# Optimization experiments

Hardware: AMD Instinct MI355X
Metric: run time of the kernel (lower is better)

The kernel has to match this reference:

```python
import jax, jax.numpy as jnp
import numpy as np

D_MODEL = 768
CODEBOOK_SIZE = 2048
CODEBOOK_DIM = 64


def setup_inputs() -> dict:
    key = jax.random.key(0)
    ks = jax.random.split(key, 10)
    B, N = 16, 4096
    h = CODEBOOK_DIM * 2  # 128
    def lin_init(k, fan_in, shape):
        bound = 1.0 / np.sqrt(fan_in)
        return jax.random.uniform(k, shape, jnp.float32, -bound, bound)
    inp = {
        "x": jax.random.normal(ks[0], (B, N, D_MODEL), jnp.float32),
        # encoder: Linear(d_model -> 2*cd), GELU, Linear(2*cd -> cd)
        "enc_w1": lin_init(ks[1], D_MODEL, (D_MODEL, h)),
        "enc_b1": lin_init(ks[2], D_MODEL, (h,)),
        "enc_w2": lin_init(ks[3], h, (h, CODEBOOK_DIM)),
        "enc_b2": lin_init(ks[4], h, (CODEBOOK_DIM,)),
        # codebook: uniform(-1/K, 1/K)
        "codebook": jax.random.uniform(ks[5], (CODEBOOK_SIZE, CODEBOOK_DIM), jnp.float32,
                                        -1.0 / CODEBOOK_SIZE, 1.0 / CODEBOOK_SIZE),
        # decoder: Linear(cd -> 2*cd), GELU, Linear(2*cd -> d_model)
        "dec_w1": lin_init(ks[6], CODEBOOK_DIM, (CODEBOOK_DIM, h)),
        "dec_b1": lin_init(ks[7], CODEBOOK_DIM, (h,)),
        "dec_w2": lin_init(ks[8], h, (h, D_MODEL)),
        "dec_b2": lin_init(ks[9], h, (D_MODEL,)),
    }
    return inp


def reference(x, enc_w1, enc_b1, enc_w2, enc_b2, codebook, dec_w1, dec_b1, dec_w2, dec_b2):
    B, N, _ = x.shape
    # encoder MLP (exact GELU, matching torch default)
    z = jax.nn.gelu(x @ enc_w1 + enc_b1, approximate=False) @ enc_w2 + enc_b2  # (B,N,cd)
    # quantize: squared-distance argmin over codebook
    flat_z = z.reshape(-1, CODEBOOK_DIM)  # (BN, cd)
    dist = (jnp.sum(flat_z * flat_z, axis=1, keepdims=True)
            + jnp.sum(codebook * codebook, axis=1)[None, :]
            - 2.0 * flat_z @ codebook.T)  # (BN, K)
    indices = jnp.argmin(dist, axis=-1)  # (BN,)
    z_q = codebook[indices].reshape(B, N, CODEBOOK_DIM)
    codebook_loss = jnp.mean((jax.lax.stop_gradient(z_q) - z) ** 2)
    embedding_loss = jnp.mean((z_q - jax.lax.stop_gradient(z)) ** 2)
    vq_loss = codebook_loss + 0.25 * embedding_loss
    # straight-through estimator
    z_q = z + jax.lax.stop_gradient(z_q - z)
    # decoder MLP
    x_rec = jax.nn.gelu(z_q @ dec_w1 + dec_b1, approximate=False) @ dec_w2 + dec_b2
    return x_rec, indices.reshape(B, N), vq_loss
```

## Files before the change

kernel.cpp:

```cpp
#include <hip/hip_runtime.h>
#include <math.h>

#define TOKENS 65536
#define DMODEL 768
#define HDIM 128
#define CDIM 64
#define NCODE 2048

__device__ __forceinline__ float gelu_exact(float v) {
    return 0.5f * v * (1.0f + erff(v * 0.7071067811865476f));
}

__device__ __forceinline__ void load_lds16(const float* g, float* l) {
    __builtin_amdgcn_global_load_lds(
        (const __attribute__((address_space(1))) void*)g,
        (__attribute__((address_space(3))) void*)l, 16, 0, 0);
}

__global__ __launch_bounds__(256) __attribute__((amdgpu_waves_per_eu(4, 4)))
void enc_fused(const float* __restrict__ x, const float* __restrict__ w1,
               const float* __restrict__ b1, const float* __restrict__ w2,
               const float* __restrict__ b2, float* __restrict__ Z)
{
    __shared__ union {
        float Wbuf[2][32][128];
        float H1s[64][132];
    } u;

    const int t = threadIdx.x;
    const int w = t >> 6, l = t & 63;
    const size_t tok0 = (size_t)blockIdx.x * 64;
    const int tg = t >> 5;
    const int cg = t & 31;

    float acc[8][4];
    #pragma unroll
    for (int i = 0; i < 8; ++i)
        #pragma unroll
        for (int j = 0; j < 4; ++j) acc[i][j] = 0.f;

    const float* xbase[8];
    #pragma unroll
    for (int i = 0; i < 8; ++i)
        xbase[i] = x + (tok0 + tg + 8 * i) * DMODEL;

    const int wrow_ = l >> 5;
    const int wcol_ = 4 * (l & 31);

    #define STAGE_W(buf, k0s)                                              \
        {                                                                  \
            float* dst = &u.Wbuf[buf][0][0];                               \
            _Pragma("unroll")                                              \
            for (int j = 0; j < 4; ++j) {                                  \
                const int chunk = w * 4 + j;                               \
                const int row = chunk * 2 + wrow_;                         \
                load_lds16(w1 + (size_t)((k0s) + row) * HDIM + wcol_,      \
                           dst + chunk * 256);                             \
            }                                                              \
        }

    STAGE_W(0, 0);
    __syncthreads();

    for (int tile = 0; tile < 24; ++tile) {
        const int k0 = tile * 32;
        const int cur = tile & 1;
        if (tile + 1 < 24) STAGE_W(cur ^ 1, k0 + 32);
        const float(*Wc)[128] = u.Wbuf[cur];
        #pragma unroll
        for (int kk = 0; kk < 32; kk += 4) {
            float4 av[8];
            #pragma unroll
            for (int i = 0; i < 8; ++i)
                av[i] = *reinterpret_cast<const float4*>(xbase[i] + k0 + kk);
            float4 bv[4];
            #pragma unroll
            for (int q = 0; q < 4; ++q)
                bv[q] = *reinterpret_cast<const float4*>(&Wc[kk + q][cg * 4]);
            #pragma unroll
            for (int i = 0; i < 8; ++i) {
                acc[i][0] = fmaf(av[i].x, bv[0].x, acc[i][0]);
                acc[i][1] = fmaf(av[i].x, bv[0].y, acc[i][1]);
                acc[i][2] = fmaf(av[i].x, bv[0].z, acc[i][2]);
                acc[i][3] = fmaf(av[i].x, bv[0].w, acc[i][3]);
                acc[i][0] = fmaf(av[i].y, bv[1].x, acc[i][0]);
                acc[i][1] = fmaf(av[i].y, bv[1].y, acc[i][1]);
                acc[i][2] = fmaf(av[i].y, bv[1].z, acc[i][2]);
                acc[i][3] = fmaf(av[i].y, bv[1].w, acc[i][3]);
                acc[i][0] = fmaf(av[i].z, bv[2].x, acc[i][0]);
                acc[i][1] = fmaf(av[i].z, bv[2].y, acc[i][1]);
                acc[i][2] = fmaf(av[i].z, bv[2].z, acc[i][2]);
                acc[i][3] = fmaf(av[i].z, bv[2].w, acc[i][3]);
                acc[i][0] = fmaf(av[i].w, bv[3].x, acc[i][0]);
                acc[i][1] = fmaf(av[i].w, bv[3].y, acc[i][1]);
                acc[i][2] = fmaf(av[i].w, bv[3].z, acc[i][2]);
                acc[i][3] = fmaf(av[i].w, bv[3].w, acc[i][3]);
            }
        }
        __syncthreads();
    }

    {
        float4 b1v = *reinterpret_cast<const float4*>(b1 + cg * 4);
        #pragma unroll
        for (int i = 0; i < 8; ++i) {
            float4 h;
            h.x = gelu_exact(acc[i][0] + b1v.x);
            h.y = gelu_exact(acc[i][1] + b1v.y);
            h.z = gelu_exact(acc[i][2] + b1v.z);
            h.w = gelu_exact(acc[i][3] + b1v.w);
            *reinterpret_cast<float4*>(&u.H1s[tg + 8 * i][cg * 4]) = h;
        }
    }
    __syncthreads();

    const int tg2 = t >> 4;
    const int cg2 = t & 15;
    const float4* w2_4 = reinterpret_cast<const float4*>(w2);
    float accB[4][4];
    #pragma unroll
    for (int i = 0; i < 4; ++i)
        #pragma unroll
        for (int j = 0; j < 4; ++j) accB[i][j] = 0.f;

    float4 bvn[4];
    #pragma unroll
    for (int q = 0; q < 4; ++q) bvn[q] = w2_4[(size_t)q * 16 + cg2];

    for (int k = 0; k < HDIM; k += 4) {
        float4 bv[4];
        #pragma unroll
        for (int q = 0; q < 4; ++q) bv[q] = bvn[q];
        if (k + 4 < HDIM) {
            #pragma unroll
            for (int q = 0; q < 4; ++q)
                bvn[q] = w2_4[(size_t)(k + 4 + q) * 16 + cg2];
        }
        float4 av[4];
        #pragma unroll
        for (int i = 0; i < 4; ++i)
            av[i] = *reinterpret_cast<const float4*>(&u.H1s[tg2 + 16 * i][k]);
        #pragma unroll
        for (int i = 0; i < 4; ++i) {
            accB[i][0] = fmaf(av[i].x, bv[0].x, accB[i][0]);
            accB[i][1] = fmaf(av[i].x, bv[0].y, accB[i][1]);
            accB[i][2] = fmaf(av[i].x, bv[0].z, accB[i][2]);
            accB[i][3] = fmaf(av[i].x, bv[0].w, accB[i][3]);
            accB[i][0] = fmaf(av[i].y, bv[1].x, accB[i][0]);
            accB[i][1] = fmaf(av[i].y, bv[1].y, accB[i][1]);
            accB[i][2] = fmaf(av[i].y, bv[1].z, accB[i][2]);
            accB[i][3] = fmaf(av[i].y, bv[1].w, accB[i][3]);
            accB[i][0] = fmaf(av[i].z, bv[2].x, accB[i][0]);
            accB[i][1] = fmaf(av[i].z, bv[2].y, accB[i][1]);
            accB[i][2] = fmaf(av[i].z, bv[2].z, accB[i][2]);
            accB[i][3] = fmaf(av[i].z, bv[2].w, accB[i][3]);
            accB[i][0] = fmaf(av[i].w, bv[3].x, accB[i][0]);
            accB[i][1] = fmaf(av[i].w, bv[3].y, accB[i][1]);
            accB[i][2] = fmaf(av[i].w, bv[3].z, accB[i][2]);
            accB[i][3] = fmaf(av[i].w, bv[3].w, accB[i][3]);
        }
    }
    {
        float4 b2v = *reinterpret_cast<const float4*>(b2 + cg2 * 4);
        #pragma unroll
        for (int i = 0; i < 4; ++i) {
            float4 o;
            o.x = accB[i][0] + b2v.x;
            o.y = accB[i][1] + b2v.y;
            o.z = accB[i][2] + b2v.z;
            o.w = accB[i][3] + b2v.w;
            *reinterpret_cast<float4*>(Z + (tok0 + tg2 + 16 * i) * CDIM + cg2 * 4) = o;
        }
    }
    #undef STAGE_W
}

__global__ __launch_bounds__(256)
void vq_kernel(const float* __restrict__ Z, const float* __restrict__ cb,
               const float* __restrict__ cnorm, int* __restrict__ idx_out,
               float* __restrict__ idxf_out, float* __restrict__ loss_accum)
{
    __shared__ float Zs[64][68];
    __shared__ float CsT[64][128];
    __shared__ float tgsum[8];

    const int t = threadIdx.x;
    const size_t tok0 = (size_t)blockIdx.x * 64;
    const int tg = t >> 5, cg = t & 31;
    const int lc = t >> 1, lh = t & 1;

    {
        int ltok = t >> 2, lq = t & 3;
        const float4* src = reinterpret_cast<const float4*>(Z + (tok0 + ltok) * CDIM + lq * 16);
        float4* dst = reinterpret_cast<float4*>(&Zs[ltok][lq * 16]);
        dst[0] = src[0]; dst[1] = src[1]; dst[2] = src[2]; dst[3] = src[3];
    }
    float4 cv[8];
    {
        const float4* src = reinterpret_cast<const float4*>(cb + (size_t)lc * CDIM + lh * 32);
        #pragma unroll
        for (int i = 0; i < 8; ++i) cv[i] = src[i];
    }
    __syncthreads();

    float zn[8];
    {
        #pragma unroll
        for (int i = 0; i < 8; ++i) {
            float a = Zs[tg + 8 * i][cg * 2];
            float b = Zs[tg + 8 * i][cg * 2 + 1];
            zn[i] = fmaf(a, a, b * b);
        }
        #pragma unroll
        for (int m = 16; m >= 1; m >>= 1)
            #pragma unroll
            for (int i = 0; i < 8; ++i) zn[i] += __shfl_xor(zn[i], m, 32);
    }

    float minv[8]; int mini[8];
    #pragma unroll
    for (int i = 0; i < 8; ++i) { minv[i] = INFINITY; mini[i] = 0; }

    for (int tile = 0; tile < 16; ++tile) {
        const int code0 = tile * 128;
        __syncthreads();
        #pragma unroll
        for (int i = 0; i < 8; ++i) {
            int k = lh * 32 + i * 4;
            CsT[k + 0][lc] = cv[i].x;
            CsT[k + 1][lc] = cv[i].y;
            CsT[k + 2][lc] = cv[i].z;
            CsT[k + 3][lc] = cv[i].w;
        }
        __syncthreads();
        if (tile + 1 < 16) {
            const float4* src = reinterpret_cast<const float4*>(
                cb + (size_t)(code0 + 128 + lc) * CDIM + lh * 32);
            #pragma unroll
            for (int i = 0; i < 8; ++i) cv[i] = src[i];
        }

        float dot[8][4];
        #pragma unroll
        for (int i = 0; i < 8; ++i)
            #pragma unroll
            for (int j = 0; j < 4; ++j) dot[i][j] = 0.f;

        #pragma unroll
        for (int k = 0; k < CDIM; k += 4) {
            float4 av[8];
            #pragma unroll
            for (int i = 0; i < 8; ++i)
                av[i] = *reinterpret_cast<const float4*>(&Zs[tg + 8 * i][k]);
            float4 bv[4];
            #pragma unroll
            for (int q = 0; q < 4; ++q)
                bv[q] = *reinterpret_cast<const float4*>(&CsT[k + q][cg * 4]);
            #pragma unroll
            for (int i = 0; i < 8; ++i) {
                dot[i][0] = fmaf(av[i].x, bv[0].x, dot[i][0]);
                dot[i][1] = fmaf(av[i].x, bv[0].y, dot[i][1]);
                dot[i][2] = fmaf(av[i].x, bv[0].z, dot[i][2]);
                dot[i][3] = fmaf(av[i].x, bv[0].w, dot[i][3]);
                dot[i][0] = fmaf(av[i].y, bv[1].x, dot[i][0]);
                dot[i][1] = fmaf(av[i].y, bv[1].y, dot[i][1]);
                dot[i][2] = fmaf(av[i].y, bv[1].z, dot[i][2]);
                dot[i][3] = fmaf(av[i].y, bv[1].w, dot[i][3]);
                dot[i][0] = fmaf(av[i].z, bv[2].x, dot[i][0]);
                dot[i][1] = fmaf(av[i].z, bv[2].y, dot[i][1]);
                dot[i][2] = fmaf(av[i].z, bv[2].z, dot[i][2]);
                dot[i][3] = fmaf(av[i].z, bv[2].w, dot[i][3]);
                dot[i][0] = fmaf(av[i].w, bv[3].x, dot[i][0]);
                dot[i][1] = fmaf(av[i].w, bv[3].y, dot[i][1]);
                dot[i][2] = fmaf(av[i].w, bv[3].z, dot[i][2]);
                dot[i][3] = fmaf(av[i].w, bv[3].w, dot[i][3]);
            }
        }
        #pragma unroll
        for (int j = 0; j < 4; ++j) {
            int ci = code0 + cg * 4 + j;
            float cn = cnorm[ci];
            #pragma unroll
            for (int i = 0; i < 8; ++i) {
                float s = (zn[i] + cn) - 2.f * dot[i][j];
                if (s < minv[i]) { minv[i] = s; mini[i] = ci; }
            }
        }
    }

    #pragma unroll
    for (int i = 0; i < 8; ++i) {
        float v = minv[i]; int ci = mini[i];
        #pragma unroll
        for (int m = 16; m >= 1; m >>= 1) {
            float ov = __shfl_xor(v, m, 32);
            int oi = __shfl_xor(ci, m, 32);
            if (ov < v || (ov == v && oi < ci)) { v = ov; ci = oi; }
        }
        minv[i] = v; mini[i] = ci;
    }

    if (cg == 0) {
        float s = 0.f;
        #pragma unroll
        for (int i = 0; i < 8; ++i) {
            size_t tok = tok0 + tg + 8 * i;
            idx_out[tok] = mini[i];
            idxf_out[tok] = (float)mini[i];
            s += minv[i];
        }
        tgsum[tg] = s;
    }
    __syncthreads();
    if (t == 0) {
        float s = 0.f;
        #pragma unroll
        for (int i = 0; i < 8; ++i) s += tgsum[i];
        atomicAdd(loss_accum, s);
    }
}

__global__ __launch_bounds__(256)
void dec1_kernel(const float* __restrict__ cb, const float* __restrict__ w1,
                 const float* __restrict__ b1, float* __restrict__ T1,
                 float* __restrict__ cnorm)
{
    __shared__ float Cs[64][68];
    __shared__ float Ws[64][128];

    const int t = threadIdx.x;
    const int c0 = blockIdx.x * 64;
    {
        int lc = t >> 2, lq = t & 3;
        const float4* src = reinterpret_cast<const float4*>(cb + (size_t)(c0 + lc) * CDIM + lq * 16);
        float4* dst = reinterpret_cast<float4*>(&Cs[lc][lq * 16]);
        dst[0] = src[0]; dst[1] = src[1]; dst[2] = src[2]; dst[3] = src[3];
    }
    #pragma unroll
    for (int i = 0; i < 8; ++i) {
        int f = t + i * 256;
        int row = f >> 5, c4 = f & 31;
        *reinterpret_cast<float4*>(&Ws[row][c4 * 4]) =
            *reinterpret_cast<const float4*>(w1 + (size_t)row * HDIM + c4 * 4);
    }
    if (t < 64) {
        const float4* p = reinterpret_cast<const float4*>(cb + (size_t)(c0 + t) * CDIM);
        float s = 0.f;
        #pragma unroll
        for (int i = 0; i < 16; ++i) {
            float4 v = p[i];
            s = fmaf(v.x, v.x, s); s = fmaf(v.y, v.y, s);
            s = fmaf(v.z, v.z, s); s = fmaf(v.w, v.w, s);
        }
        cnorm[c0 + t] = s;
    }
    __syncthreads();
    const int tg = t >> 5, cg = t & 31;
    float acc[8][4];
    #pragma unroll
    for (int i = 0; i < 8; ++i)
        #pragma unroll
        for (int j = 0; j < 4; ++j) acc[i][j] = 0.f;
    #pragma unroll
    for (int k = 0; k < CDIM; k += 4) {
        float4 av[8];
        #pragma unroll
        for (int i = 0; i < 8; ++i)
            av[i] = *reinterpret_cast<const float4*>(&Cs[tg + 8 * i][k]);
        float4 bv[4];
        #pragma unroll
        for (int q = 0; q < 4; ++q)
            bv[q] = *reinterpret_cast<const float4*>(&Ws[k + q][cg * 4]);
        #pragma unroll
        for (int i = 0; i < 8; ++i) {
            acc[i][0] = fmaf(av[i].x, bv[0].x, acc[i][0]);
            acc[i][1] = fmaf(av[i].x, bv[0].y, acc[i][1]);
            acc[i][2] = fmaf(av[i].x, bv[0].z, acc[i][2]);
            acc[i][3] = fmaf(av[i].x, bv[0].w, acc[i][3]);
            acc[i][0] = fmaf(av[i].y, bv[1].x, acc[i][0]);
            acc[i][1] = fmaf(av[i].y, bv[1].y, acc[i][1]);
            acc[i][2] = fmaf(av[i].y, bv[1].z, acc[i][2]);
            acc[i][3] = fmaf(av[i].y, bv[1].w, acc[i][3]);
            acc[i][0] = fmaf(av[i].z, bv[2].x, acc[i][0]);
            acc[i][1] = fmaf(av[i].z, bv[2].y, acc[i][1]);
            acc[i][2] = fmaf(av[i].z, bv[2].z, acc[i][2]);
            acc[i][3] = fmaf(av[i].z, bv[2].w, acc[i][3]);
            acc[i][0] = fmaf(av[i].w, bv[3].x, acc[i][0]);
            acc[i][1] = fmaf(av[i].w, bv[3].y, acc[i][1]);
            acc[i][2] = fmaf(av[i].w, bv[3].z, acc[i][2]);
            acc[i][3] = fmaf(av[i].w, bv[3].w, acc[i][3]);
        }
    }
    float4 b1v = *reinterpret_cast<const float4*>(b1 + cg * 4);
    #pragma unroll
    for (int i = 0; i < 8; ++i) {
        float4 h;
        h.x = gelu_exact(acc[i][0] + b1v.x);
        h.y = gelu_exact(acc[i][1] + b1v.y);
        h.z = gelu_exact(acc[i][2] + b1v.z);
        h.w = gelu_exact(acc[i][3] + b1v.w);
        *reinterpret_cast<float4*>(T1 + (size_t)(c0 + tg + 8 * i) * HDIM + cg * 4) = h;
    }
}

__global__ __launch_bounds__(256)
void dec2_kernel(const float* __restrict__ T1, const float* __restrict__ w2,
                 const float* __restrict__ b2, float* __restrict__ table)
{
    __shared__ float As[64][36];
    __shared__ float Ws[32][128];
    const int t = threadIdx.x;
    const int r0 = blockIdx.x * 64;
    const int col0 = blockIdx.y * 128;
    const int tg = t >> 5, cg = t & 31;
    float acc[8][4];
    #pragma unroll
    for (int i = 0; i < 8; ++i)
        #pragma unroll
        for (int j = 0; j < 4; ++j) acc[i][j] = 0.f;

    for (int k0 = 0; k0 < HDIM; k0 += 32) {
        __syncthreads();
        {
            int lr = t >> 2, lk = t & 3;
            const float4* src = reinterpret_cast<const float4*>(T1 + (size_t)(r0 + lr) * HDIM + k0 + lk * 8);
            float4 v0 = src[0], v1 = src[1];
            float4* dst = reinterpret_cast<float4*>(&As[lr][lk * 8]);
            dst[0] = v0; dst[1] = v1;
        }
        #pragma unroll
        for (int i = 0; i < 4; ++i) {
            int f = t + i * 256;
            int row = f >> 5, c4 = f & 31;
            *reinterpret_cast<float4*>(&Ws[row][c4 * 4]) =
                *reinterpret_cast<const float4*>(w2 + (size_t)(k0 + row) * DMODEL + col0 + c4 * 4);
        }
        __syncthreads();
        #pragma unroll
        for (int kk = 0; kk < 32; kk += 4) {
            float4 av[8];
            #pragma unroll
            for (int i = 0; i < 8; ++i)
                av[i] = *reinterpret_cast<const float4*>(&As[tg + 8 * i][kk]);
            float4 bv[4];
            #pragma unroll
            for (int q = 0; q < 4; ++q)
                bv[q] = *reinterpret_cast<const float4*>(&Ws[kk + q][cg * 4]);
            #pragma unroll
            for (int i = 0; i < 8; ++i) {
                acc[i][0] = fmaf(av[i].x, bv[0].x, acc[i][0]);
                acc[i][1] = fmaf(av[i].x, bv[0].y, acc[i][1]);
                acc[i][2] = fmaf(av[i].x, bv[0].z, acc[i][2]);
                acc[i][3] = fmaf(av[i].x, bv[0].w, acc[i][3]);
                acc[i][0] = fmaf(av[i].y, bv[1].x, acc[i][0]);
                acc[i][1] = fmaf(av[i].y, bv[1].y, acc[i][1]);
                acc[i][2] = fmaf(av[i].y, bv[1].z, acc[i][2]);
                acc[i][3] = fmaf(av[i].y, bv[1].w, acc[i][3]);
                acc[i][0] = fmaf(av[i].z, bv[2].x, acc[i][0]);
                acc[i][1] = fmaf(av[i].z, bv[2].y, acc[i][1]);
                acc[i][2] = fmaf(av[i].z, bv[2].z, acc[i][2]);
                acc[i][3] = fmaf(av[i].z, bv[2].w, acc[i][3]);
                acc[i][0] = fmaf(av[i].w, bv[3].x, acc[i][0]);
                acc[i][1] = fmaf(av[i].w, bv[3].y, acc[i][1]);
                acc[i][2] = fmaf(av[i].w, bv[3].z, acc[i][2]);
                acc[i][3] = fmaf(av[i].w, bv[3].w, acc[i][3]);
            }
        }
    }
    float4 b2v = *reinterpret_cast<const float4*>(b2 + col0 + cg * 4);
    #pragma unroll
    for (int i = 0; i < 8; ++i) {
        float4 o;
        o.x = acc[i][0] + b2v.x;
        o.y = acc[i][1] + b2v.y;
        o.z = acc[i][2] + b2v.z;
        o.w = acc[i][3] + b2v.w;
        *reinterpret_cast<float4*>(table + (size_t)(r0 + tg + 8 * i) * DMODEL + col0 + cg * 4) = o;
    }
}

__global__ void gather_kernel(const float* __restrict__ table,
                              const int* __restrict__ idx, float* __restrict__ out,
                              const float* __restrict__ loss_accum,
                              float* __restrict__ loss_out)
{
    if (blockIdx.x == 0 && threadIdx.x == 0) {
        loss_out[0] = loss_accum[0] * (1.25f / 4194304.0f);
    }
    const int F = TOKENS * (DMODEL / 4);
    const float4* tab4 = reinterpret_cast<const float4*>(table);
    float4* out4 = reinterpret_cast<float4*>(out);
    for (int f = blockIdx.x * blockDim.x + threadIdx.x; f < F;
         f += gridDim.x * blockDim.x) {
        int token = f / 192;
        int j = f - token * 192;
        out4[f] = tab4[(size_t)idx[token] * 192 + j];
    }
}

extern "C" void kernel_launch(void* const* d_in, const int* in_sizes, int n_in,
                              void* d_out, int out_size, void* d_ws, size_t ws_size,
                              hipStream_t stream)
{
    const float* x      = (const float*)d_in[0];
    const float* enc_w1 = (const float*)d_in[1];
    const float* enc_b1 = (const float*)d_in[2];
    const float* enc_w2 = (const float*)d_in[3];
    const float* enc_b2 = (const float*)d_in[4];
    const float* cb     = (const float*)d_in[5];
    const float* dec_w1 = (const float*)d_in[6];
    const float* dec_b1 = (const float*)d_in[7];
    const float* dec_w2 = (const float*)d_in[8];
    const float* dec_b2 = (const float*)d_in[9];

    float* out     = (float*)d_out;
    float* xrec    = out;
    float* idxf    = out + (size_t)TOKENS * DMODEL;
    float* lossout = idxf + TOKENS;

    float* ws    = (float*)d_ws;
    float* Z     = ws;
    float* T1    = Z + (size_t)TOKENS * CDIM;
    float* table = T1 + (size_t)NCODE * HDIM;
    float* cnorm = table + (size_t)NCODE * DMODEL;
    int*   idx   = (int*)(cnorm + NCODE);
    float* lacc  = (float*)(idx + TOKENS);

    hipMemsetAsync(lacc, 0, sizeof(float), stream);

    enc_fused<<<TOKENS / 64, 256, 0, stream>>>(x, enc_w1, enc_b1, enc_w2, enc_b2, Z);
    dec1_kernel<<<NCODE / 64, 256, 0, stream>>>(cb, dec_w1, dec_b1, T1, cnorm);
    dec2_kernel<<<dim3(NCODE / 64, DMODEL / 128), 256, 0, stream>>>(T1, dec_w2, dec_b2, table);
    vq_kernel<<<TOKENS / 64, 256, 0, stream>>>(Z, cb, cnorm, idx, idxf, lacc);
    gather_kernel<<<2048, 256, 0, stream>>>(table, idx, xrec, lacc, lossout);
}
```

Before: 984.6 us.

## Stage x tiles through double-buffered LDS in encoder instead of direct global reads

The encoder's first GEMM used to read x rows straight from global memory inside the inner loop. It now loads each 64x32 x tile cooperatively with coalesced float4 loads, register-prefetches the next tile, and double-buffers it in LDS next to the weight tiles. This is meant to cut uncoalesced, redundant global traffic on the dominant input stream. Row mapping changes from strided (tg+8i) to contiguous (tg*8+i) across all kernels, presumably to avoid LDS bank conflicts. The waves_per_eu hint is replaced by launch_bounds(256,3), which raises LDS use and may lower occupancy.

```diff
diff --git a/kernel.cpp b/kernel.cpp
--- a/kernel.cpp
+++ b/kernel.cpp
@@ -17,13 +17,13 @@
         (__attribute__((address_space(3))) void*)l, 16, 0, 0);
 }
 
-__global__ __launch_bounds__(256) __attribute__((amdgpu_waves_per_eu(4, 4)))
+__global__ __launch_bounds__(256, 3)
 void enc_fused(const float* __restrict__ x, const float* __restrict__ w1,
                const float* __restrict__ b1, const float* __restrict__ w2,
                const float* __restrict__ b2, float* __restrict__ Z)
 {
     __shared__ union {
-        float Wbuf[2][32][128];
+        struct { float Xs[2][64][36]; float Ws[2][32][128]; } a;
         float H1s[64][132];
     } u;
 
@@ -39,17 +39,11 @@
         #pragma unroll
         for (int j = 0; j < 4; ++j) acc[i][j] = 0.f;
 
-    const float* xbase[8];
-    #pragma unroll
-    for (int i = 0; i < 8; ++i)
-        xbase[i] = x + (tok0 + tg + 8 * i) * DMODEL;
-
     const int wrow_ = l >> 5;
     const int wcol_ = 4 * (l & 31);
-
     #define STAGE_W(buf, k0s)                                              \
         {                                                                  \
-            float* dst = &u.Wbuf[buf][0][0];                               \
+            float* dst = &u.a.Ws[buf][0][0];                               \
             _Pragma("unroll")                                              \
             for (int j = 0; j < 4; ++j) {                                  \
                 const int chunk = w * 4 + j;                               \
@@ -59,20 +53,42 @@
             }                                                              \
         }
 
+    const int ltok = t >> 2, lkg = t & 3;
+    const float* xrow = x + (tok0 + ltok) * DMODEL + lkg * 8;
+
+    float4 xr0, xr1;
+    {
+        const float4* s = reinterpret_cast<const float4*>(xrow);
+        xr0 = s[0]; xr1 = s[1];
+    }
+    *reinterpret_cast<float4*>(&u.a.Xs[0][ltok][lkg * 8]) = xr0;
+    *reinterpret_cast<float4*>(&u.a.Xs[0][ltok][lkg * 8 + 4]) = xr1;
     STAGE_W(0, 0);
+    {
+        const float4* s = reinterpret_cast<const float4*>(xrow + 32);
+        xr0 = s[0]; xr1 = s[1];
+    }
     __syncthreads();
 
     for (int tile = 0; tile < 24; ++tile) {
-        const int k0 = tile * 32;
         const int cur = tile & 1;
-        if (tile + 1 < 24) STAGE_W(cur ^ 1, k0 + 32);
-        const float(*Wc)[128] = u.Wbuf[cur];
+        if (tile + 1 < 24) {
+            *reinterpret_cast<float4*>(&u.a.Xs[cur ^ 1][ltok][lkg * 8]) = xr0;
+            *reinterpret_cast<float4*>(&u.a.Xs[cur ^ 1][ltok][lkg * 8 + 4]) = xr1;
+            STAGE_W(cur ^ 1, (tile + 1) * 32);
+            if (tile + 2 < 24) {
+                const float4* s = reinterpret_cast<const float4*>(xrow + (tile + 2) * 32);
+                xr0 = s[0]; xr1 = s[1];
+            }
+        }
+        const float(*Xc)[36] = u.a.Xs[cur];
+        const float(*Wc)[128] = u.a.Ws[cur];
         #pragma unroll
         for (int kk = 0; kk < 32; kk += 4) {
             float4 av[8];
             #pragma unroll
             for (int i = 0; i < 8; ++i)
-                av[i] = *reinterpret_cast<const float4*>(xbase[i] + k0 + kk);
+                av[i] = *reinterpret_cast<const float4*>(&Xc[tg * 8 + i][kk]);
             float4 bv[4];
             #pragma unroll
             for (int q = 0; q < 4; ++q)
@@ -109,7 +125,7 @@
             h.y = gelu_exact(acc[i][1] + b1v.y);
             h.z = gelu_exact(acc[i][2] + b1v.z);
             h.w = gelu_exact(acc[i][3] + b1v.w);
-            *reinterpret_cast<float4*>(&u.H1s[tg + 8 * i][cg * 4]) = h;
+            *reinterpret_cast<float4*>(&u.H1s[tg * 8 + i][cg * 4]) = h;
         }
     }
     __syncthreads();
@@ -139,7 +155,7 @@
         float4 av[4];
         #pragma unroll
         for (int i = 0; i < 4; ++i)
-            av[i] = *reinterpret_cast<const float4*>(&u.H1s[tg2 + 16 * i][k]);
+            av[i] = *reinterpret_cast<const float4*>(&u.H1s[tg2 * 4 + i][k]);
         #pragma unroll
         for (int i = 0; i < 4; ++i) {
             accB[i][0] = fmaf(av[i].x, bv[0].x, accB[i][0]);
@@ -169,7 +185,7 @@
             o.y = accB[i][1] + b2v.y;
             o.z = accB[i][2] + b2v.z;
             o.w = accB[i][3] + b2v.w;
-            *reinterpret_cast<float4*>(Z + (tok0 + tg2 + 16 * i) * CDIM + cg2 * 4) = o;
+            *reinterpret_cast<float4*>(Z + (tok0 + tg2 * 4 + i) * CDIM + cg2 * 4) = o;
         }
     }
     #undef STAGE_W
@@ -207,8 +223,8 @@
     {
         #pragma unroll
         for (int i = 0; i < 8; ++i) {
-            float a = Zs[tg + 8 * i][cg * 2];
-            float b = Zs[tg + 8 * i][cg * 2 + 1];
+            float a = Zs[tg * 8 + i][cg * 2];
+            float b = Zs[tg * 8 + i][cg * 2 + 1];
             zn[i] = fmaf(a, a, b * b);
         }
         #pragma unroll
@@ -251,7 +267,7 @@
             float4 av[8];
             #pragma unroll
             for (int i = 0; i < 8; ++i)
-                av[i] = *reinterpret_cast<const float4*>(&Zs[tg + 8 * i][k]);
+                av[i] = *reinterpret_cast<const float4*>(&Zs[tg * 8 + i][k]);
             float4 bv[4];
             #pragma unroll
             for (int q = 0; q < 4; ++q)
@@ -304,7 +320,7 @@
         float s = 0.f;
         #pragma unroll
         for (int i = 0; i < 8; ++i) {
-            size_t tok = tok0 + tg + 8 * i;
+            size_t tok = tok0 + tg * 8 + i;
             idx_out[tok] = mini[i];
             idxf_out[tok] = (float)mini[i];
             s += minv[i];
@@ -366,7 +382,7 @@
         float4 av[8];
         #pragma unroll
         for (int i = 0; i < 8; ++i)
-            av[i] = *reinterpret_cast<const float4*>(&Cs[tg + 8 * i][k]);
+            av[i] = *reinterpret_cast<const float4*>(&Cs[tg * 8 + i][k]);
         float4 bv[4];
         #pragma unroll
         for (int q = 0; q < 4; ++q)
@@ -399,7 +415,7 @@
         h.y = gelu_exact(acc[i][1] + b1v.y);
         h.z = gelu_exact(acc[i][2] + b1v.z);
         h.w = gelu_exact(acc[i][3] + b1v.w);
-        *reinterpret_cast<float4*>(T1 + (size_t)(c0 + tg + 8 * i) * HDIM + cg * 4) = h;
+        *reinterpret_cast<float4*>(T1 + (size_t)(c0 + tg * 8 + i) * HDIM + cg * 4) = h;
     }
 }
 
@@ -441,7 +457,7 @@
             float4 av[8];
             #pragma unroll
             for (int i = 0; i < 8; ++i)
-                av[i] = *reinterpret_cast<const float4*>(&As[tg + 8 * i][kk]);
+                av[i] = *reinterpret_cast<const float4*>(&As[tg * 8 + i][kk]);
             float4 bv[4];
             #pragma unroll
             for (int q = 0; q < 4; ++q)
@@ -475,7 +491,7 @@
         o.y = acc[i][1] + b2v.y;
         o.z = acc[i][2] + b2v.z;
         o.w = acc[i][3] + b2v.w;
-        *reinterpret_cast<float4*>(table + (size_t)(r0 + tg + 8 * i) * DMODEL + col0 + cg * 4) = o;
+        *reinterpret_cast<float4*>(table + (size_t)(r0 + tg * 8 + i) * DMODEL + col0 + cg * 4) = o;
     }
 }
 
```

Measured after the change: 844.5 us. -14.2%, faster.
